# Optimization experiments

Measured on AMD Instinct MI355X. Metric: run time of the kernel, lower is better.

Reference implementation:

```python
import jax, jax.numpy as jnp
import numpy as np
from jax import lax

C = 64
RED = 8
BN_EPS = 1e-5

def _conv1x1(x, W, b):
    # x: [N,C,H,W], W: [O,C] (1x1 conv kernel squeezed), b: [O]
    return jnp.einsum('nchw,oc->nohw', x, W) + b[None, :, None, None]

def _cross_attention(img, depth, Wq, bq, Wk, bk, Wv, bv, gamma):
    # img, depth: [N,C,H,W]; channel-channel attention (attn is [N,C,C])
    N, c, H, Wd = img.shape
    HW = H * Wd
    q = _conv1x1(img, Wq, bq).reshape(N, c, HW).astype(jnp.float32)
    k = _conv1x1(depth, Wk, bk).reshape(N, c, HW).astype(jnp.float32)
    v = _conv1x1(depth, Wv, bv).reshape(N, c, HW).astype(jnp.float32)
    attn = jax.nn.softmax(jnp.einsum('nci,ndi->ncd', q, k), axis=-1)  # [N,C,C]
    out = jnp.einsum('ncd,ndi->nci', attn, v).reshape(N, c, H, Wd).astype(img.dtype)
    return gamma * out + img

def _mlp(x, w1, b1, w2, b2):
    h = jax.nn.relu(x @ w1.T + b1)
    return h @ w2.T + b2

def _cbam(x, fc1_w, fc1_b, fc2_w, fc2_b, sa_w, sa_b):
    # x: [N,C,H,W]
    avg = x.mean(axis=(2, 3))          # [N,C]
    mx = x.max(axis=(2, 3))            # [N,C]
    ch = jax.nn.sigmoid(_mlp(avg, fc1_w, fc1_b, fc2_w, fc2_b)
                        + _mlp(mx, fc1_w, fc1_b, fc2_w, fc2_b))  # [N,C]
    x = x * ch[:, :, None, None]
    sp_in = jnp.stack([x.mean(axis=1), x.max(axis=1)], axis=1)   # [N,2,H,W]
    sp = lax.conv_general_dilated(sp_in, sa_w, (1, 1), 'SAME',
                                  dimension_numbers=('NCHW', 'OIHW', 'NCHW')) + sa_b[None, :, None, None]
    return x * jax.nn.sigmoid(sp)


def setup_inputs() -> dict:
    key = jax.random.key(0)
    ks = jax.random.split(key, 20)
    B, S, H, W = 2, 8, 128, 128
    s = 0.05
    d = {
        'img_feat': jax.random.normal(ks[0], (B, S, C, H, W), jnp.float32),
        'depth_feat': jax.random.normal(ks[1], (B, S, C, H, W), jnp.float32),
        # CrossAttention (shared module, used for both directions)
        'Wq': jax.random.normal(ks[2], (C, C), jnp.float32) * s,
        'bq': jax.random.normal(ks[3], (C,), jnp.float32) * s,
        'Wk': jax.random.normal(ks[4], (C, C), jnp.float32) * s,
        'bk': jax.random.normal(ks[5], (C,), jnp.float32) * s,
        'Wv': jax.random.normal(ks[6], (C, C), jnp.float32) * s,
        'bv': jax.random.normal(ks[7], (C,), jnp.float32) * s,
        'gamma': jax.random.normal(ks[8], (1,), jnp.float32) * 0.5,
        # fusion conv (3x3, 2C -> C) + BN (inference, running stats)
        'Wf': jax.random.normal(ks[9], (C, 2 * C, 3, 3), jnp.float32) * s,
        'bf': jax.random.normal(ks[10], (C,), jnp.float32) * s,
        'bn_g': jnp.ones((C,), jnp.float32),
        'bn_b': jnp.zeros((C,), jnp.float32),
        'bn_m': jax.random.normal(ks[11], (C,), jnp.float32) * s,
        'bn_v': jax.random.uniform(ks[12], (C,), jnp.float32, 0.5, 1.5),
        # CBAM channel MLP + spatial conv (7x7, 2 -> 1)
        'fc1_w': jax.random.normal(ks[13], (C // RED, C), jnp.float32) * s,
        'fc1_b': jax.random.normal(ks[14], (C // RED,), jnp.float32) * s,
        'fc2_w': jax.random.normal(ks[15], (C, C // RED), jnp.float32) * s,
        'fc2_b': jax.random.normal(ks[16], (C,), jnp.float32) * s,
        'sa_w': jax.random.normal(ks[17], (1, 2, 7, 7), jnp.float32) * s,
        'sa_b': jax.random.normal(ks[18], (1,), jnp.float32) * s,
    }
    return d


def reference(img_feat, depth_feat, Wq, bq, Wk, bk, Wv, bv, gamma,
              Wf, bf, bn_g, bn_b, bn_m, bn_v,
              fc1_w, fc1_b, fc2_w, fc2_b, sa_w, sa_b):
    B, S, c, H, W = img_feat.shape
    img = img_feat.reshape(-1, c, H, W)
    dep = depth_feat.reshape(-1, c, H, W)
    img_att = _cross_attention(img, dep, Wq, bq, Wk, bk, Wv, bv, gamma)
    dep_att = _cross_attention(dep, img, Wq, bq, Wk, bk, Wv, bv, gamma)
    fused = jnp.concatenate([img_att, dep_att], axis=1)  # [N,2C,H,W]
    fused = lax.conv_general_dilated(fused, Wf, (1, 1), 'SAME',
                                     dimension_numbers=('NCHW', 'OIHW', 'NCHW')) + bf[None, :, None, None]
    inv = bn_g * lax.rsqrt(bn_v + BN_EPS)
    fused = jax.nn.relu(fused * inv[None, :, None, None] + (bn_b - bn_m * inv)[None, :, None, None])
    fused = _cbam(fused, fc1_w, fc1_b, fc2_w, fc2_b, sa_w, sa_b)
    return fused.reshape(B, S, c, H, W)
```

## Files before the change

kernel.cpp:

```cpp
#include <hip/hip_runtime.h>
#include <math.h>


typedef __bf16 bf16_t;
typedef bf16_t bf16x8 __attribute__((ext_vector_type(8)));
typedef bf16_t bf16x4 __attribute__((ext_vector_type(4)));
typedef float  f32x4  __attribute__((ext_vector_type(4)));
typedef _Float16 f16_t;
typedef f16_t  f16x8  __attribute__((ext_vector_type(8)));

static constexpr int  CH  = 64;
static constexpr int  H   = 128;
static constexpr int  W   = 128;
static constexpr int  HW  = H * W;
static constexpr int  NI  = 16;
static constexpr int  NCK = 16;

static constexpr int W_WQ=0, W_BQ=4096, W_WK=4160, W_BK=8256, W_WV=8320, W_BV=12416,
  W_GAMMA=12480, W_WF=12481, W_BF=86209, W_BNG=86273, W_BNB=86337, W_BNM=86401,
  W_BNV=86465, W_FC1W=86529, W_FC1B=87041, W_FC2W=87049, W_FC2B=87561,
  W_SAW=87625, W_SAB=87723, W_TOTAL=87724;

static constexpr size_t OFF_GPART  = 0;
static constexpr size_t SZ_GPART   = (size_t)NI*NCK*4096*4;
static constexpr size_t OFF_SX     = OFF_GPART + SZ_GPART;
static constexpr size_t SZ_SXY     = (size_t)NI*NCK*64*4;
static constexpr size_t OFF_SY     = OFF_SX + SZ_SXY;
static constexpr size_t OFF_M1     = OFF_SY + SZ_SXY;
static constexpr size_t SZ_M       = (size_t)NI*4096*4;
static constexpr size_t OFF_M2     = OFF_M1 + SZ_M;
static constexpr size_t OFF_T1     = OFF_M2 + SZ_M;
static constexpr size_t SZ_T       = (size_t)NI*64*4;
static constexpr size_t OFF_T2     = OFF_T1 + SZ_T;
static constexpr size_t OFF_BCONST = OFF_T2 + SZ_T;
static constexpr size_t OFF_WH     = OFF_BCONST + 256;
static constexpr size_t SZ_WH      = (size_t)NI*64*9*128*2;
static constexpr size_t OFF_WINDT  = OFF_WH + SZ_WH;
static constexpr size_t SZ_WIND    = (size_t)NI*9*64*4;
static constexpr size_t OFF_IND    = OFF_WINDT + SZ_WIND;
static constexpr size_t OFF_BSUM   = OFF_IND + SZ_WIND;
static constexpr size_t SZ_BST     = (size_t)NI*64*64*4;
static constexpr size_t OFF_BMAX   = OFF_BSUM + SZ_BST;
static constexpr size_t OFF_CHS    = OFF_BMAX + SZ_BST;
static constexpr size_t OFF_SPIN   = OFF_CHS + SZ_T;
static constexpr size_t SZ_SPIN    = (size_t)NI*2*HW*4;
static constexpr size_t OFF_FLAG   = OFF_SPIN + SZ_SPIN;
static constexpr size_t OFF_WF32   = OFF_FLAG + 256;
static constexpr size_t OFF_P16    = ((OFF_WF32 + (size_t)W_TOTAL*4 + 255) / 256) * 256;
static constexpr size_t SZ_P16     = (size_t)NI*4*HW*32*2;

__global__ __launch_bounds__(256) void k0_detect(
    const unsigned short* __restrict__ u, int* __restrict__ flag)
{
  __shared__ int bad;
  if (threadIdx.x == 0) bad = 0;
  __syncthreads();
  int local = 0;
  for (int i = threadIdx.x; i < 4096; i += 256) {
    const unsigned short v = u[2*i];
    const int e = (v >> 7) & 0xFF;
    if (e >= 0xC0) local = 1;
  }
  if (local) atomicOr(&bad, 1);
  __syncthreads();
  if (threadIdx.x == 0) flag[0] = bad;
}

struct WPack { const void* p[19]; int sz[19]; int off[19]; };

__global__ __launch_bounds__(256) void kw_convert(
    WPack wp, const int* __restrict__ flag, float* __restrict__ dst)
{
  const int j = blockIdx.y;
  const int i = blockIdx.x * 256 + threadIdx.x;
  if (i >= wp.sz[j]) return;
  const int f32m = flag[0];
  float v;
  if (f32m) v = ((const float*)wp.p[j])[i];
  else      v = (float)((const bf16_t*)wp.p[j])[i];
  dst[wp.off[j] + i] = v;
}

__global__ __launch_bounds__(256) void kc_pack(
    const bf16_t* __restrict__ Xb, const bf16_t* __restrict__ Yb,
    const float* __restrict__ Xf, const float* __restrict__ Yf,
    const int* __restrict__ flag, f16_t* __restrict__ P16)
{
  const int lin = blockIdx.x * 256 + threadIdx.x;
  const int oct = lin & 3;
  const int p   = (lin >> 2) & 16383;
  const int s   = (lin >> 16) & 3;
  const int n   = lin >> 18;
  const int f32m = flag[0];
  const size_t nbase = (size_t)n * CH * HW;
  const int c0 = (s & 1) * 32 + oct * 8;
  const float*  Fsrc = (s < 2) ? Xf : Yf;
  const bf16_t* Bsrc = (s < 2) ? Xb : Yb;
  f16x8 h;
  #pragma unroll
  for (int j = 0; j < 8; ++j) {
    const size_t q = nbase + (size_t)(c0 + j) * HW + p;
    const float v = f32m ? Fsrc[q] : (float)Bsrc[q];
    h[j] = (f16_t)v;
  }
  *(f16x8*)(P16 + (size_t)lin * 8) = h;
}

__global__ __launch_bounds__(256) void k1_gram(
    const bf16_t* __restrict__ Xb, const bf16_t* __restrict__ Yb,
    const float* __restrict__ Xf, const float* __restrict__ Yf,
    const int* __restrict__ flag,
    float* __restrict__ Gpart, float* __restrict__ sxpart, float* __restrict__ sypart)
{
  const int chunk = blockIdx.x, n = blockIdx.y;
  const int t = threadIdx.x, lane = t & 63, wv = t >> 6;
  const int mrow = lane & 15, quad = lane >> 4;
  const int f32m = flag[0];
  const size_t nbase = (size_t)n * CH * HW;
  const int p0 = chunk * 1024 + wv * 256;

  f32x4 acc[4][4], acc2[4][4];
  #pragma unroll
  for (int i = 0; i < 4; ++i)
    #pragma unroll
    for (int j = 0; j < 4; ++j) {
      acc[i][j]  = (f32x4){0.f, 0.f, 0.f, 0.f};
      acc2[i][j] = (f32x4){0.f, 0.f, 0.f, 0.f};
    }
  float sxl[4] = {0.f,0.f,0.f,0.f}, syl[4] = {0.f,0.f,0.f,0.f};

  for (int kt = 0; kt < 8; ++kt) {
    const int pk = p0 + kt * 32 + quad * 8;
    if (f32m) {
      bf16x8 a[4], b[4], al[4], bl[4];
      #pragma unroll
      for (int mt = 0; mt < 4; ++mt) {
        const size_t ia = nbase + (size_t)(mt*16 + mrow) * HW + pk;
        float sa = 0.f, sb = 0.f;
        #pragma unroll
        for (int j = 0; j < 8; ++j) {
          const float va = Xf[ia + j];
          const bf16_t ha = (bf16_t)va;
          a[mt][j] = ha; al[mt][j] = (bf16_t)(va - (float)ha); sa += va;
          const float vb = Yf[ia + j];
          const bf16_t hb = (bf16_t)vb;
          b[mt][j] = hb; bl[mt][j] = (bf16_t)(vb - (float)hb); sb += vb;
        }
        sxl[mt] += sa; syl[mt] += sb;
      }
      #pragma unroll
      for (int mt = 0; mt < 4; ++mt)
        #pragma unroll
        for (int nt = 0; nt < 4; ++nt) {
          acc[mt][nt]  = __builtin_amdgcn_mfma_f32_16x16x32_bf16(a[mt],  b[nt],  acc[mt][nt],  0, 0, 0);
          acc2[mt][nt] = __builtin_amdgcn_mfma_f32_16x16x32_bf16(a[mt],  bl[nt], acc2[mt][nt], 0, 0, 0);
          acc2[mt][nt] = __builtin_amdgcn_mfma_f32_16x16x32_bf16(al[mt], b[nt],  acc2[mt][nt], 0, 0, 0);
        }
    } else {
      bf16x8 a[4], b[4];
      #pragma unroll
      for (int mt = 0; mt < 4; ++mt) {
        const size_t ia = nbase + (size_t)(mt*16 + mrow) * HW + pk;
        a[mt] = *(const bf16x8*)(Xb + ia);
        b[mt] = *(const bf16x8*)(Yb + ia);
        float sa = 0.f, sb = 0.f;
        #pragma unroll
        for (int j = 0; j < 8; ++j) { sa += (float)a[mt][j]; sb += (float)b[mt][j]; }
        sxl[mt] += sa; syl[mt] += sb;
      }
      #pragma unroll
      for (int mt = 0; mt < 4; ++mt)
        #pragma unroll
        for (int nt = 0; nt < 4; ++nt)
          acc[mt][nt] = __builtin_amdgcn_mfma_f32_16x16x32_bf16(a[mt], b[nt], acc[mt][nt], 0, 0, 0);
    }
  }

  #pragma unroll
  for (int mt = 0; mt < 4; ++mt) {
    sxl[mt] += __shfl_xor(sxl[mt], 16, 64); sxl[mt] += __shfl_xor(sxl[mt], 32, 64);
    syl[mt] += __shfl_xor(syl[mt], 16, 64); syl[mt] += __shfl_xor(syl[mt], 32, 64);
  }

  __shared__ float Gs[4096];
  __shared__ float sxs[64], sys[64];
  for (int w2 = 0; w2 < 4; ++w2) {
    if (wv == w2) {
      #pragma unroll
      for (int mt = 0; mt < 4; ++mt) {
        #pragma unroll
        for (int nt = 0; nt < 4; ++nt) {
          #pragma unroll
          for (int r = 0; r < 4; ++r) {
            const int c = mt*16 + quad*4 + r, d = nt*16 + mrow;
            const float val = acc[mt][nt][r] + acc2[mt][nt][r];
            if (w2 == 0) Gs[c*64 + d]  = val;
            else         Gs[c*64 + d] += val;
          }
        }
        if (quad == 0) {
          const int c = mt*16 + mrow;
          if (w2 == 0) { sxs[c] = sxl[mt];  sys[c] = syl[mt]; }
          else         { sxs[c] += sxl[mt]; sys[c] += syl[mt]; }
        }
      }
    }
    __syncthreads();
  }
  float* Gp = Gpart + ((size_t)n*NCK + chunk) * 4096;
  for (int i = t; i < 4096; i += 256) Gp[i] = Gs[i];
  if (t < 64)       sxpart[((size_t)n*NCK + chunk)*64 + t]        = sxs[t];
  else if (t < 128) sypart[((size_t)n*NCK + chunk)*64 + (t - 64)] = sys[t - 64];
}

__global__ __launch_bounds__(256) void k2a_attn(
    const float* __restrict__ Gpart, const float* __restrict__ sxpart, const float* __restrict__ sypart,
    const float* __restrict__ wt,
    float* __restrict__ M1, float* __restrict__ M2,
    float* __restrict__ T1, float* __restrict__ T2)
{
  const int n = blockIdx.x, t = threadIdx.x;
  __shared__ float Gs[4096], Gts[4160];
  __shared__ float P1s[4096], P2s[4096];
  __shared__ float A1s[4160], A2s[4160];
  __shared__ float sxs[64], sys[64], ux[64], uy[64], vx[64], vy[64];

  for (int i = t; i < 4096; i += 256) {
    float s = 0.f;
    for (int c2 = 0; c2 < NCK; ++c2) s += Gpart[((size_t)n*NCK + c2)*4096 + i];
    Gs[i] = s;
    Gts[(i & 63)*65 + (i >> 6)] = s;
  }
  if (t < 64) {
    float s = 0.f; for (int c2 = 0; c2 < NCK; ++c2) s += sxpart[((size_t)n*NCK + c2)*64 + t];
    sxs[t] = s;
  } else if (t < 128) {
    const int c = t - 64;
    float s = 0.f; for (int c2 = 0; c2 < NCK; ++c2) s += sypart[((size_t)n*NCK + c2)*64 + c];
    sys[c] = s;
  }
  __syncthreads();

  for (int i = t; i < 4096; i += 256) {
    const int c = i >> 6, e = i & 63;
    float s1 = 0.f, s2 = 0.f;
    for (int a = 0; a < 64; ++a) {
      const float w = wt[W_WQ + c*64 + a];
      s1 += w * Gs[a*64 + e];
      s2 += w * Gts[a*65 + e];
    }
    P1s[i] = s1; P2s[i] = s2;
  }
  {
    const int which = t >> 6, c = t & 63;
    float s = 0.f;
    if (which == 0)      { for (int a = 0; a < 64; ++a) s += wt[W_WQ + c*64+a]*sxs[a]; ux[c] = s; }
    else if (which == 1) { for (int a = 0; a < 64; ++a) s += wt[W_WQ + c*64+a]*sys[a]; uy[c] = s; }
    else if (which == 2) { for (int a = 0; a < 64; ++a) s += wt[W_WK + c*64+a]*sxs[a]; vx[c] = s; }
    else                 { for (int a = 0; a < 64; ++a) s += wt[W_WK + c*64+a]*sys[a]; vy[c] = s; }
  }
  __syncthreads();

  for (int i = t; i < 4096; i += 256) {
    const int c = i >> 6, d = i & 63;
    float s1 = 0.f, s2 = 0.f;
    for (int e = 0; e < 64; ++e) {
      const float wk = wt[W_WK + d*64 + e];
      s1 += P1s[c*64 + e] * wk;
      s2 += P2s[c*64 + e] * wk;
    }
    const float bqc = wt[W_BQ + c], bkd = wt[W_BK + d];
    s1 += ux[c]*bkd + bqc*vy[d] + 16384.f*bqc*bkd;
    s2 += uy[c]*bkd + bqc*vx[d] + 16384.f*bqc*bkd;
    A1s[c*65 + d] = s1; A2s[c*65 + d] = s2;
  }
  __syncthreads();

  if (t < 128) {
    float* R = (t < 64) ? (A1s + (t)*65) : (A2s + (t - 64)*65);
    float m = R[0];
    for (int d = 1; d < 64; ++d) m = fmaxf(m, R[d]);
    float s = 0.f;
    for (int d = 0; d < 64; ++d) { const float e2 = expf(R[d] - m); R[d] = e2; s += e2; }
    const float inv = 1.f / s;
    for (int d = 0; d < 64; ++d) R[d] *= inv;
  }
  __syncthreads();

  for (int i = t; i < 4096; i += 256) {
    const int c = i >> 6, e = i & 63;
    float s1 = 0.f, s2 = 0.f;
    for (int d = 0; d < 64; ++d) {
      const float wv = wt[W_WV + d*64 + e];
      s1 += A1s[c*65 + d] * wv;
      s2 += A2s[c*65 + d] * wv;
    }
    M1[(size_t)n*4096 + i] = s1;
    M2[(size_t)n*4096 + i] = s2;
  }
  if (t < 64) {
    float s1 = 0.f, s2 = 0.f;
    for (int d = 0; d < 64; ++d) {
      const float b = wt[W_BV + d];
      s1 += A1s[t*65 + d] * b;
      s2 += A2s[t*65 + d] * b;
    }
    T1[n*64 + t] = s1; T2[n*64 + t] = s2;
  }
}

__global__ __launch_bounds__(256) void k2b_weff(
    const float* __restrict__ wt,
    const float* __restrict__ M1, const float* __restrict__ M2,
    const float* __restrict__ T1, const float* __restrict__ T2,
    f16_t* __restrict__ Wh, float* __restrict__ windT, float* __restrict__ bconst)
{
  const int tap = blockIdx.x, dir = blockIdx.y, n = blockIdx.z;
  const int t = threadIdx.x;
  const float g = wt[W_GAMMA];
  f16_t* Whn = Wh + (size_t)n * 64 * 9 * 128;
  const float* Mo = (dir == 0) ? (M2 + (size_t)n*4096) : (M1 + (size_t)n*4096);

  __shared__ float Wfs[8192];
  __shared__ float Ms[4096];

  #pragma unroll
  for (int i = t; i < 8192; i += 256) Wfs[i] = wt[W_WF + i*9 + tap];
  for (int i = t; i < 4096; i += 256) Ms[i] = Mo[i];
  __syncthreads();

  const int e = t & 63;
  const int coff = dir ? 0 : 64;
  const int boff = dir ? 64 : 0;
  #pragma unroll 4
  for (int it = 0; it < 16; ++it) {
    const int o = (t >> 6) + 4*it;
    const float inv = wt[W_BNG + o] * rsqrtf(wt[W_BNV + o] + 1e-5f);
    const float base = Wfs[o*128 + boff + e];
    float s = 0.f;
    #pragma unroll 8
    for (int c = 0; c < 64; ++c)
      s += Wfs[o*128 + coff + c] * Ms[c*64 + e];
    Whn[(o*9 + tap)*128 + dir*64 + e] = (f16_t)(inv * (base + g * s));
  }

  if (dir == 0 && t < 64) {
    const int o = t;
    const float inv = wt[W_BNG + o] * rsqrtf(wt[W_BNV + o] + 1e-5f);
    float s = 0.f;
    for (int c = 0; c < 64; ++c)
      s += wt[W_WF + (o*128 + c)*9 + tap]      * T1[n*64 + c]
         + wt[W_WF + (o*128 + 64 + c)*9 + tap] * T2[n*64 + c];
    windT[((size_t)n*9 + tap)*64 + o] = inv * g * s;
    if (tap == 0 && n == 0)
      bconst[o] = wt[W_BF + o]*inv + wt[W_BNB + o] - wt[W_BNM + o]*inv;
  }
}

__global__ __launch_bounds__(64) void k2c_ind(
    const float* __restrict__ windT, float* __restrict__ ind)
{
  const int n = blockIdx.x, o = threadIdx.x;
  float w9[9];
  #pragma unroll
  for (int tp = 0; tp < 9; ++tp) w9[tp] = windT[((size_t)n*9 + tp)*64 + o];
  #pragma unroll
  for (int yc = 0; yc < 3; ++yc) {
    const int ky0 = (yc == 0) ? 1 : 0, ky1 = (yc == 2) ? 1 : 2;
    #pragma unroll
    for (int xc = 0; xc < 3; ++xc) {
      const int kx0 = (xc == 0) ? 1 : 0, kx1 = (xc == 2) ? 1 : 2;
      float s = 0.f;
      for (int ky = ky0; ky <= ky1; ++ky)
        for (int kx = kx0; kx <= kx1; ++kx) s += w9[ky*3 + kx];
      ind[((size_t)n*9 + yc*3 + xc)*64 + o] = s;
    }
  }
}

__global__ __launch_bounds__(256) void k3_conv(
    const bf16_t* __restrict__ Xb, const bf16_t* __restrict__ Yb,
    const float* __restrict__ Xf, const float* __restrict__ Yf,
    const int* __restrict__ flag,
    const f16_t* __restrict__ Wh, const float* __restrict__ bconst,
    const float* __restrict__ ind,
    const f16_t* __restrict__ P16, const int useP16,
    bf16_t* __restrict__ fusedB, float* __restrict__ fusedF,
    float* __restrict__ bsum, float* __restrict__ bmax)
{
  __shared__ __attribute__((aligned(16))) f16_t sbuf[4][130][40];
  __shared__ float sind[576], sconst[64];
  __shared__ float ssum[4][64], smax[4][64];
  const int rp = blockIdx.x, n = blockIdx.y;
  const int t = threadIdx.x, lane = t & 63, wv = t >> 6;
  const int l15 = lane & 15, quad = lane >> 4;
  const int ly = wv >> 1, ch2 = wv & 1;
  const int f32m = flag[0];
  const size_t nbase = (size_t)n * CH * HW;
  const f16_t* __restrict__ Whn = Wh + (size_t)n * 64 * 9 * 128;

  for (int i = t; i < 576; i += 256) sind[i] = ind[(size_t)n*576 + i];
  if (t < 64) sconst[t] = bconst[t];
  {
    const int r = t >> 6, cs = (t >> 5) & 1, sl = t & 31;
    sbuf[r][cs ? 129 : 0][sl] = (f16_t)0.f;
  }

  f32x4 acc[4][4];
  #pragma unroll
  for (int i = 0; i < 4; ++i)
    #pragma unroll
    for (int j = 0; j < 4; ++j) acc[i][j] = (f32x4){0.f, 0.f, 0.f, 0.f};

  if (useP16) {
    const int oct = t & 3;
    const int sl  = t >> 2;
    const f16_t* __restrict__ PnB = P16 + (size_t)(n*4) * HW * 32;
    f16x8 h[8];

    #define K3_STAGE_LOAD(S)                                                  \
      { const f16_t* __restrict__ Pn = PnB + (size_t)(S) * HW * 32;           \
        _Pragma("unroll")                                                     \
        for (int i = 0; i < 8; ++i) {                                         \
          const int r  = i >> 1;                                              \
          const int x  = (i & 1) * 64 + sl;                                   \
          const int gy = rp*2 - 1 + r;                                        \
          f16x8 v;                                                            \
          _Pragma("unroll")                                                   \
          for (int k2 = 0; k2 < 8; ++k2) v[k2] = (f16_t)0.f;                  \
          if (gy >= 0 && gy < H)                                              \
            v = *(const f16x8*)(Pn + ((size_t)(gy*128 + x) * 32 + oct*8));    \
          h[i] = v;                                                           \
        } }
    #define K3_STAGE_WRITE()                                                  \
      { _Pragma("unroll")                                                     \
        for (int i = 0; i < 8; ++i) {                                         \
          const int r    = i >> 1;                                            \
          const int colL = (i & 1) * 64 + sl + 1;                             \
          *(f16x8*)&sbuf[r][colL][(oct ^ (colL & 3)) * 8] = h[i];             \
        } }

    K3_STAGE_LOAD(0)
    K3_STAGE_WRITE()
    for (int s = 0; s < 4; ++s) {
      if (s < 3) K3_STAGE_LOAD(s + 1)
      asm volatile("s_waitcnt lgkmcnt(0)" ::: "memory");
      __builtin_amdgcn_s_barrier();
      __builtin_amdgcn_s_setprio(1);
      #pragma unroll
      for (int tap = 0; tap < 9; ++tap) {
        const int ky = tap / 3, kx = tap % 3;
        f16x8 bfr[4];
        #pragma unroll
        for (int nt = 0; nt < 4; ++nt) {
          const int o = nt*16 + l15;
          bfr[nt] = *(const f16x8*)(Whn + ((o*9 + tap)*128 + s*32 + quad*8));
        }
        f16x8 afr[4];
        const int row = ly + ky;
        #pragma unroll
        for (int mt = 0; mt < 4; ++mt) {
          const int col = ch2*64 + mt*16 + l15 + kx;
          afr[mt] = *(const f16x8*)&sbuf[row][col][(quad ^ (col & 3)) * 8];
        }
        #pragma unroll
        for (int mt = 0; mt < 4; ++mt)
          #pragma unroll
          for (int nt = 0; nt < 4; ++nt)
            acc[mt][nt] = __builtin_amdgcn_mfma_f32_16x16x32_f16(afr[mt], bfr[nt], acc[mt][nt], 0, 0, 0);
      }
      __builtin_amdgcn_s_setprio(0);
      __builtin_amdgcn_s_barrier();
      if (s < 3) K3_STAGE_WRITE()
    }
    #undef K3_STAGE_LOAD
    #undef K3_STAGE_WRITE
  } else {
    const int cstage = t & 127, rsel = t >> 7;
    for (int s = 0; s < 4; ++s) {
      __syncthreads();
      #pragma unroll
      for (int pass = 0; pass < 2; ++pass) {
        const int r = rsel + 2*pass;
        const int gy = rp*2 - 1 + r;
        const bool valid = (gy >= 0) && (gy < H);
        const int colL = cstage + 1;
        #pragma unroll
        for (int oct = 0; oct < 4; ++oct) {
          f16x8 hh;
          #pragma unroll
          for (int j = 0; j < 8; ++j) {
            const int g = s*32 + oct*8 + j;
            float v = 0.f;
            if (valid) {
              const size_t q = nbase + (size_t)(g & 63)*HW + gy*W + cstage;
              v = (g < 64) ? (f32m ? Xf[q] : (float)Xb[q])
                           : (f32m ? Yf[q] : (float)Yb[q]);
            }
            hh[j] = (f16_t)v;
          }
          *(f16x8*)&sbuf[r][colL][(oct ^ (colL & 3)) * 8] = hh;
        }
      }
      __syncthreads();
      #pragma unroll
      for (int tap = 0; tap < 9; ++tap) {
        const int ky = tap / 3, kx = tap % 3;
        f16x8 bfr[4];
        #pragma unroll
        for (int nt = 0; nt < 4; ++nt) {
          const int o = nt*16 + l15;
          bfr[nt] = *(const f16x8*)(Whn + ((o*9 + tap)*128 + s*32 + quad*8));
        }
        f16x8 afr[4];
        const int row = ly + ky;
        #pragma unroll
        for (int mt = 0; mt < 4; ++mt) {
          const int col = ch2*64 + mt*16 + l15 + kx;
          afr[mt] = *(const f16x8*)&sbuf[row][col][(quad ^ (col & 3)) * 8];
        }
        #pragma unroll
        for (int mt = 0; mt < 4; ++mt)
          #pragma unroll
          for (int nt = 0; nt < 4; ++nt)
            acc[mt][nt] = __builtin_amdgcn_mfma_f32_16x16x32_f16(afr[mt], bfr[nt], acc[mt][nt], 0, 0, 0);
      }
    }
  }

  const int y = rp*2 + ly;
  const int yc = (y == 0) ? 0 : (y == H-1) ? 2 : 1;
  #pragma unroll
  for (int nt = 0; nt < 4; ++nt) {
    const int o = nt*16 + l15;
    const float bc = sconst[o];
    float ssm = 0.f, smx = 0.f;
    #pragma unroll
    for (int mt = 0; mt < 4; ++mt) {
      const int xb = ch2*64 + mt*16 + quad*4;
      f32x4 vals;
      #pragma unroll
      for (int r = 0; r < 4; ++r) {
        const int x = xb + r;
        const int xc = (x == 0) ? 0 : (x == W-1) ? 2 : 1;
        float v = acc[mt][nt][r] + bc + sind[(yc*3 + xc)*64 + o];
        v = fmaxf(v, 0.f);
        vals[r] = v; ssm += v; smx = fmaxf(smx, v);
      }
      const size_t off = nbase + (size_t)o*HW + y*W + xb;
      if (f32m) {
        *(f32x4*)(fusedF + off) = vals;
      } else {
        bf16x4 pv;
        #pragma unroll
        for (int r = 0; r < 4; ++r) pv[r] = (bf16_t)vals[r];
        *(bf16x4*)(fusedB + off) = pv;
      }
    }
    ssm += __shfl_xor(ssm, 16, 64); ssm += __shfl_xor(ssm, 32, 64);
    smx = fmaxf(smx, __shfl_xor(smx, 16, 64));
    smx = fmaxf(smx, __shfl_xor(smx, 32, 64));
    if (quad == 0) { ssum[wv][o] = ssm; smax[wv][o] = smx; }
  }
  __syncthreads();
  if (t < 64) {
    const float S = ssum[0][t] + ssum[1][t] + ssum[2][t] + ssum[3][t];
    const float M = fmaxf(fmaxf(smax[0][t], smax[1][t]), fmaxf(smax[2][t], smax[3][t]));
    bsum[((size_t)n*64 + rp)*64 + t] = S;
    bmax[((size_t)n*64 + rp)*64 + t] = M;
  }
}

__global__ __launch_bounds__(64) void k4_chgate(
    const float* __restrict__ bsum, const float* __restrict__ bmax,
    const float* __restrict__ wt, float* __restrict__ chout)
{
  const int n = blockIdx.x, t = threadIdx.x;
  __shared__ float avg[64], mxs[64], h1[8], h2[8];
  float S = 0.f, M = 0.f;
  for (int rp = 0; rp < 64; ++rp) {
    S += bsum[((size_t)n*64 + rp)*64 + t];
    M = fmaxf(M, bmax[((size_t)n*64 + rp)*64 + t]);
  }
  avg[t] = S * (1.f / 16384.f);
  mxs[t] = M;
  __syncthreads();
  if (t < 8) {
    float s = wt[W_FC1B + t];
    for (int c = 0; c < 64; ++c) s += wt[W_FC1W + t*64 + c] * avg[c];
    h1[t] = fmaxf(s, 0.f);
  } else if (t < 16) {
    const int r = t - 8;
    float s = wt[W_FC1B + r];
    for (int c = 0; c < 64; ++c) s += wt[W_FC1W + r*64 + c] * mxs[c];
    h2[r] = fmaxf(s, 0.f);
  }
  __syncthreads();
  float s = 2.f * wt[W_FC2B + t];
  for (int r = 0; r < 8; ++r) s += wt[W_FC2W + t*8 + r] * (h1[r] + h2[r]);
  chout[n*64 + t] = 1.f / (1.f + expf(-s));
}

__global__ __launch_bounds__(256) void k5_spin(
    const bf16_t* __restrict__ fusedB, const float* __restrict__ fusedF,
    const int* __restrict__ flag,
    const float* __restrict__ chs, float* __restrict__ spin)
{
  const int n = blockIdx.y;
  const int p0 = (blockIdx.x * 256 + threadIdx.x) * 8;
  const int f32m = flag[0];
  const size_t nbase = (size_t)n * CH * HW;
  const float* c = chs + n * 64;
  float s[8], m[8];
  #pragma unroll
  for (int k = 0; k < 8; ++k) { s[k] = 0.f; m[k] = 0.f; }
  if (f32m) {
    for (int o = 0; o < 64; ++o) {
      const float co = c[o];
      const float* q = fusedF + nbase + (size_t)o*HW + p0;
      const f32x4 a = *(const f32x4*)q;
      const f32x4 b = *(const f32x4*)(q + 4);
      #pragma unroll
      for (int k = 0; k < 4; ++k) {
        const float v0 = a[k] * co; s[k]   += v0; m[k]   = fmaxf(m[k],   v0);
        const float v1 = b[k] * co; s[4+k] += v1; m[4+k] = fmaxf(m[4+k], v1);
      }
    }
  } else {
    for (int o = 0; o < 64; ++o) {
      const float co = c[o];
      const bf16x8 a = *(const bf16x8*)(fusedB + nbase + (size_t)o*HW + p0);
      #pragma unroll
      for (int k = 0; k < 8; ++k) {
        const float v = (float)a[k] * co; s[k] += v; m[k] = fmaxf(m[k], v);
      }
    }
  }
  f32x4 o0, o1, o2, o3;
  #pragma unroll
  for (int k = 0; k < 4; ++k) {
    o0[k] = s[k]   * (1.f / 64.f);
    o1[k] = s[4+k] * (1.f / 64.f);
    o2[k] = m[k];
    o3[k] = m[4+k];
  }
  *(f32x4*)(spin + (size_t)n*2*HW + p0)          = o0;
  *(f32x4*)(spin + (size_t)n*2*HW + p0 + 4)      = o1;
  *(f32x4*)(spin + (size_t)n*2*HW + HW + p0)     = o2;
  *(f32x4*)(spin + (size_t)n*2*HW + HW + p0 + 4) = o3;
}

__global__ __launch_bounds__(256) void k6_final(
    bf16_t* __restrict__ fusedB, float* __restrict__ fusedF,
    const int* __restrict__ flag,
    const float* __restrict__ chs, const float* __restrict__ spin,
    const float* __restrict__ wt)
{
  const int n = blockIdx.y;
  const int p0 = (blockIdx.x * 256 + threadIdx.x) * 8;
  const int y = p0 >> 7, x0 = p0 & 127;
  const int f32m = flag[0];
  const float* s0 = spin + (size_t)n*2*HW;
  const float* s1 = s0 + HW;
  float acc[8];
  {
    const float sab = wt[W_SAB];
    #pragma unroll
    for (int k = 0; k < 8; ++k) acc[k] = sab;
  }
  for (int j = 0; j < 7; ++j) {
    const int yy = y + j - 3;
    if (yy < 0 || yy >= H) continue;
    const float* r0 = s0 + yy*W;
    const float* r1 = s1 + yy*W;
    float v0[14], v1[14];
    #pragma unroll
    for (int ii = 0; ii < 14; ++ii) {
      const int xx = x0 + ii - 3;
      const bool ok = (xx >= 0) && (xx < W);
      v0[ii] = ok ? r0[xx] : 0.f;
      v1[ii] = ok ? r1[xx] : 0.f;
    }
    #pragma unroll
    for (int i = 0; i < 7; ++i) {
      const float w0 = wt[W_SAW + j*7 + i];
      const float w1 = wt[W_SAW + 49 + j*7 + i];
      #pragma unroll
      for (int k = 0; k < 8; ++k)
        acc[k] += w0 * v0[i+k] + w1 * v1[i+k];
    }
  }
  float sp[8];
  #pragma unroll
  for (int k = 0; k < 8; ++k) sp[k] = 1.f / (1.f + expf(-acc[k]));
  const size_t nbase = (size_t)n * CH * HW;
  const float* c = chs + n * 64;
  if (f32m) {
    for (int o = 0; o < 64; ++o) {
      const float co = c[o];
      float* q = fusedF + nbase + (size_t)o*HW + p0;
      f32x4 a = *(f32x4*)q;
      f32x4 b = *(f32x4*)(q + 4);
      #pragma unroll
      for (int k = 0; k < 4; ++k) {
        a[k] = a[k] * co * sp[k];
        b[k] = b[k] * co * sp[4+k];
      }
      *(f32x4*)q       = a;
      *(f32x4*)(q + 4) = b;
    }
  } else {
    for (int o = 0; o < 64; ++o) {
      const float co = c[o];
      bf16_t* q = fusedB + nbase + (size_t)o*HW + p0;
      bf16x8 a = *(bf16x8*)q;
      #pragma unroll
      for (int k = 0; k < 8; ++k)
        a[k] = (bf16_t)((float)a[k] * co * sp[k]);
      *(bf16x8*)q = a;
    }
  }
}

extern "C" void kernel_launch(void* const* d_in, const int* in_sizes, int n_in,
                              void* d_out, int out_size, void* d_ws, size_t ws_size,
                              hipStream_t stream)
{
  (void)n_in; (void)out_size; (void)in_sizes;
  char* ws = (char*)d_ws;
  float*  Gpart  = (float*)(ws + OFF_GPART);
  float*  sxp    = (float*)(ws + OFF_SX);
  float*  syp    = (float*)(ws + OFF_SY);
  float*  M1     = (float*)(ws + OFF_M1);
  float*  M2     = (float*)(ws + OFF_M2);
  float*  T1     = (float*)(ws + OFF_T1);
  float*  T2     = (float*)(ws + OFF_T2);
  float*  bconst = (float*)(ws + OFF_BCONST);
  f16_t*  Wh     = (f16_t*)(ws + OFF_WH);
  float*  windT  = (float*)(ws + OFF_WINDT);
  float*  indt   = (float*)(ws + OFF_IND);
  float*  bsum   = (float*)(ws + OFF_BSUM);
  float*  bmax   = (float*)(ws + OFF_BMAX);
  float*  chs    = (float*)(ws + OFF_CHS);
  float*  spin   = (float*)(ws + OFF_SPIN);
  int*    flag   = (int*)  (ws + OFF_FLAG);
  float*  wf32   = (float*)(ws + OFF_WF32);
  f16_t*  P16    = (f16_t*)(ws + OFF_P16);
  bf16_t* fusedB = (bf16_t*)d_out;
  float*  fusedF = (float*)d_out;

  const int useP16 = (ws_size >= OFF_P16 + SZ_P16) ? 1 : 0;

  const bf16_t* imgB = (const bf16_t*)d_in[0];
  const bf16_t* depB = (const bf16_t*)d_in[1];
  const float*  imgF = (const float*) d_in[0];
  const float*  depF = (const float*) d_in[1];

  WPack wp;
  static const int wsz[19] = {4096,64,4096,64,4096,64,1,73728,64,64,64,64,64,512,8,512,64,98,1};
  static const int woff[19] = {W_WQ,W_BQ,W_WK,W_BK,W_WV,W_BV,W_GAMMA,W_WF,W_BF,W_BNG,
                               W_BNB,W_BNM,W_BNV,W_FC1W,W_FC1B,W_FC2W,W_FC2B,W_SAW,W_SAB};
  for (int j = 0; j < 19; ++j) { wp.p[j] = d_in[2 + j]; wp.sz[j] = wsz[j]; wp.off[j] = woff[j]; }

  hipLaunchKernelGGL(k0_detect, dim3(1), dim3(256), 0, stream,
                     (const unsigned short*)d_in[0], flag);
  hipLaunchKernelGGL(kw_convert, dim3(288, 19), dim3(256), 0, stream, wp, flag, wf32);
  if (useP16)
    hipLaunchKernelGGL(kc_pack, dim3(16384), dim3(256), 0, stream,
                       imgB, depB, imgF, depF, flag, P16);
  hipLaunchKernelGGL(k1_gram,  dim3(NCK, NI), dim3(256), 0, stream,
                     imgB, depB, imgF, depF, flag, Gpart, sxp, syp);
  hipLaunchKernelGGL(k2a_attn, dim3(NI), dim3(256), 0, stream,
                     Gpart, sxp, syp, wf32, M1, M2, T1, T2);
  hipLaunchKernelGGL(k2b_weff, dim3(9, 2, NI), dim3(256), 0, stream,
                     wf32, M1, M2, T1, T2, Wh, windT, bconst);
  hipLaunchKernelGGL(k2c_ind,  dim3(NI), dim3(64), 0, stream, windT, indt);
  hipLaunchKernelGGL(k3_conv,  dim3(64, NI), dim3(256), 0, stream,
                     imgB, depB, imgF, depF, flag, Wh, bconst, indt,
                     P16, useP16, fusedB, fusedF, bsum, bmax);
  hipLaunchKernelGGL(k4_chgate, dim3(NI), dim3(64), 0, stream,
                     bsum, bmax, wf32, chs);
  hipLaunchKernelGGL(k5_spin,  dim3(8, NI), dim3(256), 0, stream,
                     fusedB, fusedF, flag, chs, spin);
  hipLaunchKernelGGL(k6_final, dim3(8, NI), dim3(256), 0, stream,
                     fusedB, fusedF, flag, chs, spin, wf32);
}
```

Before: 503.5 us.

## Stage attention weights in LDS and register-block small matmuls in attn/weff kernels

The attention kernel now copies Wq/Wk/Wv into padded shared memory and keeps one operand column in registers, so each thread computes 16 outputs with vectorized LDS reads instead of re-reading global weights in scalar inner loops. The transposed Gram copy is dropped and read through registers instead. The weight-conversion kernel also writes a tap-major transposed copy of the fusion conv weight, so k2b_weff can load it with coalesced vector loads instead of stride-9 gathers. This targets the small serial per-sample kernels, at the cost of more LDS and registers (launch bounds of 1 block per CU) and an extra workspace buffer.

```diff
diff --git a/kernel.cpp b/kernel.cpp
--- a/kernel.cpp
+++ b/kernel.cpp
@@ -46,7 +46,9 @@
 static constexpr size_t SZ_SPIN    = (size_t)NI*2*HW*4;
 static constexpr size_t OFF_FLAG   = OFF_SPIN + SZ_SPIN;
 static constexpr size_t OFF_WF32   = OFF_FLAG + 256;
-static constexpr size_t OFF_P16    = ((OFF_WF32 + (size_t)W_TOTAL*4 + 255) / 256) * 256;
+static constexpr size_t OFF_WFT    = ((OFF_WF32 + (size_t)W_TOTAL*4 + 255) / 256) * 256;
+static constexpr size_t SZ_WFT     = (size_t)9*8192*4;
+static constexpr size_t OFF_P16    = ((OFF_WFT + SZ_WFT + 255) / 256) * 256;
 static constexpr size_t SZ_P16     = (size_t)NI*4*HW*32*2;
 
 __global__ __launch_bounds__(256) void k0_detect(
@@ -69,7 +71,8 @@
 struct WPack { const void* p[19]; int sz[19]; int off[19]; };
 
 __global__ __launch_bounds__(256) void kw_convert(
-    WPack wp, const int* __restrict__ flag, float* __restrict__ dst)
+    WPack wp, const int* __restrict__ flag, float* __restrict__ dst,
+    float* __restrict__ WFT)
 {
   const int j = blockIdx.y;
   const int i = blockIdx.x * 256 + threadIdx.x;
@@ -79,6 +82,7 @@
   if (f32m) v = ((const float*)wp.p[j])[i];
   else      v = (float)((const bf16_t*)wp.p[j])[i];
   dst[wp.off[j] + i] = v;
+  if (j == 7) WFT[(i % 9) * 8192 + (i / 9)] = v;
 }
 
 __global__ __launch_bounds__(256) void kc_pack(
@@ -213,23 +217,31 @@
   else if (t < 128) sypart[((size_t)n*NCK + chunk)*64 + (t - 64)] = sys[t - 64];
 }
 
-__global__ __launch_bounds__(256) void k2a_attn(
+__global__ __launch_bounds__(256, 1) void k2a_attn(
     const float* __restrict__ Gpart, const float* __restrict__ sxpart, const float* __restrict__ sypart,
     const float* __restrict__ wt,
     float* __restrict__ M1, float* __restrict__ M2,
     float* __restrict__ T1, float* __restrict__ T2)
 {
   const int n = blockIdx.x, t = threadIdx.x;
-  __shared__ float Gs[4096], Gts[4160];
+  constexpr int SW = 68;
+  __shared__ float Gs[4096];
   __shared__ float P1s[4096], P2s[4096];
-  __shared__ float A1s[4160], A2s[4160];
+  __shared__ float A1s[64*SW], A2s[64*SW];
+  __shared__ float WQs[64*SW], WKs[64*SW], WVs[64*SW];
   __shared__ float sxs[64], sys[64], ux[64], uy[64], vx[64], vy[64];
 
   for (int i = t; i < 4096; i += 256) {
-    float s = 0.f;
-    for (int c2 = 0; c2 < NCK; ++c2) s += Gpart[((size_t)n*NCK + c2)*4096 + i];
-    Gs[i] = s;
-    Gts[(i & 63)*65 + (i >> 6)] = s;
+    const int r = i >> 6, cc = i & 63;
+    WQs[r*SW + cc] = wt[W_WQ + i];
+    WKs[r*SW + cc] = wt[W_WK + i];
+    WVs[r*SW + cc] = wt[W_WV + i];
+  }
+  for (int i4 = t; i4 < 1024; i4 += 256) {
+    f32x4 s = (f32x4){0.f, 0.f, 0.f, 0.f};
+    for (int c2 = 0; c2 < NCK; ++c2)
+      s += *(const f32x4*)(Gpart + ((size_t)n*NCK + c2)*4096 + i4*4);
+    *(f32x4*)(Gs + i4*4) = s;
   }
   if (t < 64) {
     float s = 0.f; for (int c2 = 0; c2 < NCK; ++c2) s += sxpart[((size_t)n*NCK + c2)*64 + t];
@@ -241,43 +253,73 @@
   }
   __syncthreads();
 
-  for (int i = t; i < 4096; i += 256) {
-    const int c = i >> 6, e = i & 63;
-    float s1 = 0.f, s2 = 0.f;
-    for (int a = 0; a < 64; ++a) {
-      const float w = wt[W_WQ + c*64 + a];
-      s1 += w * Gs[a*64 + e];
-      s2 += w * Gts[a*65 + e];
-    }
-    P1s[i] = s1; P2s[i] = s2;
+  {
+    const int e = t & 63;
+    float Greg[64], GTreg[64];
+    #pragma unroll
+    for (int a = 0; a < 64; ++a) Greg[a] = Gs[a*64 + e];
+    #pragma unroll
+    for (int a4 = 0; a4 < 16; ++a4)
+      *(f32x4*)(GTreg + a4*4) = *(const f32x4*)(Gs + e*64 + a4*4);
+    for (int it = 0; it < 16; ++it) {
+      const int c = (t >> 6) + 4*it;
+      float s1 = 0.f, s2 = 0.f;
+      #pragma unroll
+      for (int a4 = 0; a4 < 16; ++a4) {
+        const f32x4 w4 = *(const f32x4*)(WQs + c*SW + a4*4);
+        #pragma unroll
+        for (int r = 0; r < 4; ++r) {
+          s1 += w4[r] * Greg[a4*4 + r];
+          s2 += w4[r] * GTreg[a4*4 + r];
+        }
+      }
+      P1s[c*64 + e] = s1; P2s[c*64 + e] = s2;
+    }
   }
   {
     const int which = t >> 6, c = t & 63;
+    const float* Wrow = (which < 2) ? (WQs + c*SW) : (WKs + c*SW);
+    const float* vecv = ((which & 1) == 0) ? sxs : sys;
     float s = 0.f;
-    if (which == 0)      { for (int a = 0; a < 64; ++a) s += wt[W_WQ + c*64+a]*sxs[a]; ux[c] = s; }
-    else if (which == 1) { for (int a = 0; a < 64; ++a) s += wt[W_WQ + c*64+a]*sys[a]; uy[c] = s; }
-    else if (which == 2) { for (int a = 0; a < 64; ++a) s += wt[W_WK + c*64+a]*sxs[a]; vx[c] = s; }
-    else                 { for (int a = 0; a < 64; ++a) s += wt[W_WK + c*64+a]*sys[a]; vy[c] = s; }
-  }
-  __syncthreads();
-
-  for (int i = t; i < 4096; i += 256) {
-    const int c = i >> 6, d = i & 63;
-    float s1 = 0.f, s2 = 0.f;
-    for (int e = 0; e < 64; ++e) {
-      const float wk = wt[W_WK + d*64 + e];
-      s1 += P1s[c*64 + e] * wk;
-      s2 += P2s[c*64 + e] * wk;
-    }
-    const float bqc = wt[W_BQ + c], bkd = wt[W_BK + d];
-    s1 += ux[c]*bkd + bqc*vy[d] + 16384.f*bqc*bkd;
-    s2 += uy[c]*bkd + bqc*vx[d] + 16384.f*bqc*bkd;
-    A1s[c*65 + d] = s1; A2s[c*65 + d] = s2;
+    #pragma unroll
+    for (int a = 0; a < 64; ++a) s += Wrow[a] * vecv[a];
+    if      (which == 0) ux[c] = s;
+    else if (which == 1) uy[c] = s;
+    else if (which == 2) vx[c] = s;
+    else                 vy[c] = s;
+  }
+  __syncthreads();
+
+  {
+    const int d = t & 63;
+    float WKreg[64];
+    #pragma unroll
+    for (int a4 = 0; a4 < 16; ++a4)
+      *(f32x4*)(WKreg + a4*4) = *(const f32x4*)(WKs + d*SW + a4*4);
+    const float bkd = wt[W_BK + d];
+    for (int it = 0; it < 16; ++it) {
+      const int c = (t >> 6) + 4*it;
+      float s1 = 0.f, s2 = 0.f;
+      #pragma unroll
+      for (int e4 = 0; e4 < 16; ++e4) {
+        const f32x4 p1 = *(const f32x4*)(P1s + c*64 + e4*4);
+        const f32x4 p2 = *(const f32x4*)(P2s + c*64 + e4*4);
+        #pragma unroll
+        for (int r = 0; r < 4; ++r) {
+          s1 += p1[r] * WKreg[e4*4 + r];
+          s2 += p2[r] * WKreg[e4*4 + r];
+        }
+      }
+      const float bqc = wt[W_BQ + c];
+      s1 += ux[c]*bkd + bqc*vy[d] + 16384.f*bqc*bkd;
+      s2 += uy[c]*bkd + bqc*vx[d] + 16384.f*bqc*bkd;
+      A1s[c*SW + d] = s1; A2s[c*SW + d] = s2;
+    }
   }
   __syncthreads();
 
   if (t < 128) {
-    float* R = (t < 64) ? (A1s + (t)*65) : (A2s + (t - 64)*65);
+    float* R = (t < 64) ? (A1s + t*SW) : (A2s + (t - 64)*SW);
     float m = R[0];
     for (int d = 1; d < 64; ++d) m = fmaxf(m, R[d]);
     float s = 0.f;
@@ -287,30 +329,41 @@
   }
   __syncthreads();
 
-  for (int i = t; i < 4096; i += 256) {
-    const int c = i >> 6, e = i & 63;
-    float s1 = 0.f, s2 = 0.f;
-    for (int d = 0; d < 64; ++d) {
-      const float wv = wt[W_WV + d*64 + e];
-      s1 += A1s[c*65 + d] * wv;
-      s2 += A2s[c*65 + d] * wv;
-    }
-    M1[(size_t)n*4096 + i] = s1;
-    M2[(size_t)n*4096 + i] = s2;
+  {
+    const int e = t & 63;
+    float WVreg[64];
+    #pragma unroll
+    for (int dd = 0; dd < 64; ++dd) WVreg[dd] = WVs[dd*SW + e];
+    for (int it = 0; it < 16; ++it) {
+      const int c = (t >> 6) + 4*it;
+      float s1 = 0.f, s2 = 0.f;
+      #pragma unroll
+      for (int d4 = 0; d4 < 16; ++d4) {
+        const f32x4 a1 = *(const f32x4*)(A1s + c*SW + d4*4);
+        const f32x4 a2 = *(const f32x4*)(A2s + c*SW + d4*4);
+        #pragma unroll
+        for (int r = 0; r < 4; ++r) {
+          s1 += a1[r] * WVreg[d4*4 + r];
+          s2 += a2[r] * WVreg[d4*4 + r];
+        }
+      }
+      M1[(size_t)n*4096 + c*64 + e] = s1;
+      M2[(size_t)n*4096 + c*64 + e] = s2;
+    }
   }
   if (t < 64) {
     float s1 = 0.f, s2 = 0.f;
     for (int d = 0; d < 64; ++d) {
       const float b = wt[W_BV + d];
-      s1 += A1s[t*65 + d] * b;
-      s2 += A2s[t*65 + d] * b;
+      s1 += A1s[t*SW + d] * b;
+      s2 += A2s[t*SW + d] * b;
     }
     T1[n*64 + t] = s1; T2[n*64 + t] = s2;
   }
 }
 
 __global__ __launch_bounds__(256) void k2b_weff(
-    const float* __restrict__ wt,
+    const float* __restrict__ wt, const float* __restrict__ WFT,
     const float* __restrict__ M1, const float* __restrict__ M2,
     const float* __restrict__ T1, const float* __restrict__ T2,
     f16_t* __restrict__ Wh, float* __restrict__ windT, float* __restrict__ bconst)
@@ -324,23 +377,29 @@
   __shared__ float Wfs[8192];
   __shared__ float Ms[4096];
 
-  #pragma unroll
-  for (int i = t; i < 8192; i += 256) Wfs[i] = wt[W_WF + i*9 + tap];
-  for (int i = t; i < 4096; i += 256) Ms[i] = Mo[i];
+  for (int i4 = t; i4 < 2048; i4 += 256)
+    *(f32x4*)(Wfs + i4*4) = *(const f32x4*)(WFT + (size_t)tap*8192 + i4*4);
+  for (int i4 = t; i4 < 1024; i4 += 256)
+    *(f32x4*)(Ms + i4*4) = *(const f32x4*)(Mo + i4*4);
   __syncthreads();
 
   const int e = t & 63;
+  float Msreg[64];
+  #pragma unroll
+  for (int c = 0; c < 64; ++c) Msreg[c] = Ms[c*64 + e];
   const int coff = dir ? 0 : 64;
   const int boff = dir ? 64 : 0;
-  #pragma unroll 4
   for (int it = 0; it < 16; ++it) {
     const int o = (t >> 6) + 4*it;
     const float inv = wt[W_BNG + o] * rsqrtf(wt[W_BNV + o] + 1e-5f);
     const float base = Wfs[o*128 + boff + e];
     float s = 0.f;
-    #pragma unroll 8
-    for (int c = 0; c < 64; ++c)
-      s += Wfs[o*128 + coff + c] * Ms[c*64 + e];
+    #pragma unroll
+    for (int c4 = 0; c4 < 16; ++c4) {
+      const f32x4 w4 = *(const f32x4*)(Wfs + o*128 + coff + c4*4);
+      #pragma unroll
+      for (int r = 0; r < 4; ++r) s += w4[r] * Msreg[c4*4 + r];
+    }
     Whn[(o*9 + tap)*128 + dir*64 + e] = (f16_t)(inv * (base + g * s));
   }
 
@@ -745,6 +804,7 @@
   float*  spin   = (float*)(ws + OFF_SPIN);
   int*    flag   = (int*)  (ws + OFF_FLAG);
   float*  wf32   = (float*)(ws + OFF_WF32);
+  float*  wft    = (float*)(ws + OFF_WFT);
   f16_t*  P16    = (f16_t*)(ws + OFF_P16);
   bf16_t* fusedB = (bf16_t*)d_out;
   float*  fusedF = (float*)d_out;
@@ -764,7 +824,7 @@
 
   hipLaunchKernelGGL(k0_detect, dim3(1), dim3(256), 0, stream,
                      (const unsigned short*)d_in[0], flag);
-  hipLaunchKernelGGL(kw_convert, dim3(288, 19), dim3(256), 0, stream, wp, flag, wf32);
+  hipLaunchKernelGGL(kw_convert, dim3(288, 19), dim3(256), 0, stream, wp, flag, wf32, wft);
   if (useP16)
     hipLaunchKernelGGL(kc_pack, dim3(16384), dim3(256), 0, stream,
                        imgB, depB, imgF, depF, flag, P16);
@@ -773,7 +833,7 @@
   hipLaunchKernelGGL(k2a_attn, dim3(NI), dim3(256), 0, stream,
                      Gpart, sxp, syp, wf32, M1, M2, T1, T2);
   hipLaunchKernelGGL(k2b_weff, dim3(9, 2, NI), dim3(256), 0, stream,
-                     wf32, M1, M2, T1, T2, Wh, windT, bconst);
+                     wf32, wft, M1, M2, T1, T2, Wh, windT, bconst);
   hipLaunchKernelGGL(k2c_ind,  dim3(NI), dim3(64), 0, stream, windT, indt);
   hipLaunchKernelGGL(k3_conv,  dim3(64, NI), dim3(256), 0, stream,
                      imgB, depB, imgF, depF, flag, Wh, bconst, indt,
```

Result: faster. 447.8 us (-11.1%).
